# Kernel optimization log

Hardware: AMD Instinct MI355X
Metric: run time of the kernel (lower is better)

Reference implementation:

```python
import jax, jax.numpy as jnp
import numpy as np

B, N, DIM = 16, 1024, 768


def setup_inputs() -> dict:
    key = jax.random.key(0)
    ks = jax.random.split(key, 8)
    x = jax.random.normal(ks[0], (B, N, DIM), dtype=jnp.float32)
    y = jax.random.normal(ks[1], (B, N, DIM), dtype=jnp.float32)
    coords = jax.random.normal(ks[2], (N, N, 6), dtype=jnp.float32)
    # orthogonal init for U (as in torch init.orthogonal_)
    a = jax.random.normal(ks[3], (DIM, DIM), dtype=jnp.float32)
    q, r = jnp.linalg.qr(a)
    U = q * jnp.sign(jnp.diagonal(r))[None, :]
    S1 = jnp.ones((DIM,), dtype=jnp.float32)
    S2 = jnp.ones((DIM,), dtype=jnp.float32)
    gating = jnp.asarray(1.0, dtype=jnp.float32)
    temp = jnp.asarray(0.1, dtype=jnp.float32)
    pos_emb = jnp.zeros((N, 6, 1), dtype=jnp.float32)
    return {"x": x, "y": y, "coords": coords, "U": U, "S1": S1, "S2": S2,
            "gating": gating, "temp": temp, "pos_emb": pos_emb}


def reference(x, y, coords, U, S1, S2, gating, temp, pos_emb):
    dim = x.shape[-1]
    scale = dim ** (-0.5)
    # spectral decomposition: x @ U^T @ diag(S^2) @ U
    xu = x @ U.T                                   # [B,N,d]
    x1 = (xu * jnp.square(S1)) @ U                 # [B,N,d]
    x2 = (xu * jnp.square(S2)) @ U                 # [B,N,d]
    xs = jnp.stack([x1, x2], axis=1)               # [B,2,N,d]
    patch_score = jax.nn.softmax(
        jnp.einsum('bknd,bmd->bknm', xs, y) * scale, axis=-1)  # [B,2,N,M]
    pos = jnp.squeeze(coords @ pos_emb, -1)        # [N,M]
    pos_score = jax.nn.softmax(pos, axis=-1)[None, None]        # [1,1,N,M]
    g = jax.nn.sigmoid(gating)
    attn = (1.0 - g) * patch_score + g * pos_score  # [B,2,N,M]
    # entropy-routed gating
    entropy = jnp.sum(-attn * jnp.log(attn + 1e-8), axis=-1)    # [B,2,N]
    hmap = 2.0 - 2.0 * jax.nn.sigmoid(temp * jnp.transpose(entropy, (0, 2, 1)))  # [B,N,2]
    fgbg = hmap[..., 0] >= hmap[..., 1]
    route = jax.lax.stop_gradient(
        jnp.stack([fgbg, ~fgbg], axis=-1).astype(hmap.dtype))   # [B,N,2]
    heat_map = jnp.sum(hmap * route, axis=-1, keepdims=True)    # [B,N,1]
    attn_c = jnp.sum(attn * jnp.transpose(route, (0, 2, 1))[..., None], axis=1)  # [B,N,M]
    out = attn_c @ y                               # [B,N,d]
    return (out, heat_map)
```

## Files before the change

### kernel.cpp

```cpp
#include <hip/hip_runtime.h>
#include <hip/hip_bf16.h>

#define DEV __device__ __forceinline__

typedef unsigned short u16;
typedef short short8 __attribute__((ext_vector_type(8)));
typedef u16 u16x4 __attribute__((ext_vector_type(4)));
typedef float f32x16 __attribute__((ext_vector_type(16)));

static const int BB = 16;
static const int NN = 1024;
static const int DD = 768;

DEV u16 f2bf(float f) {
    unsigned u = __builtin_bit_cast(unsigned, f);
    unsigned r = u + 0x7fffu + ((u >> 16) & 1u);
    return (u16)(r >> 16);
}
DEV float h2f(u16 u) { return (float)__builtin_bit_cast(_Float16, u); }
DEV u16 f2h(float f) { return __builtin_bit_cast(u16, (_Float16)f); }

DEV void gl_lds16(const void* g, void* l) {
    __builtin_amdgcn_global_load_lds(
        (const __attribute__((address_space(1))) unsigned int*)g,
        (__attribute__((address_space(3))) unsigned int*)l, 16, 0, 0);
}

DEV void fence_bar() {
    asm volatile("" ::: "memory");
    __builtin_amdgcn_s_barrier();
    asm volatile("" ::: "memory");
}
DEV void wait_vm4() { asm volatile("s_waitcnt vmcnt(4)" ::: "memory"); }

template<int OM>
__global__ __launch_bounds__(256, 3) void gemm128(
    const u16* __restrict__ Ag, const u16* __restrict__ Bg, void* __restrict__ Cg,
    int K, int N, int zmod,
    long sA0, long sA1, long sB0, long sB1, long sC0, long sC1,
    float scale)
{
    __shared__ u16 As[128 * 64];
    __shared__ u16 Bs[128 * 64];

    int z = blockIdx.z;
    const u16* A = Ag + (long)(z % zmod) * sA0 + (long)(z / zmod) * sA1;
    const u16* B = Bg + (long)(z % zmod) * sB0 + (long)(z / zmod) * sB1;
    u16*   Cu = (u16*)Cg   + (long)(z % zmod) * sC0 + (long)(z / zmod) * sC1;
    float* Cf = (float*)Cg + (long)(z % zmod) * sC0 + (long)(z / zmod) * sC1;

    int tid  = threadIdx.x;
    int lane = tid & 63, wave = tid >> 6;
    int wm = wave & 1, wn = wave >> 1;
    int ln31 = lane & 31, khalf = lane >> 5;

    long m0 = (long)blockIdx.x * 128;
    long n0 = (long)blockIdx.y * 128;

    long aOfs[4], bOfs[4];
    u16 *lA[4], *lB[4];
#pragma unroll
    for (int i = 0; i < 4; i++) {
        int p = tid + i * 256;
        int row = p >> 3, qs = p & 7;
        int q = qs ^ (row & 7);
        aOfs[i] = (m0 + row) * (long)K + q * 8;
        bOfs[i] = (n0 + row) * (long)K + q * 8;
        lA[i] = As + p * 8;
        lB[i] = Bs + p * 8;
    }

    int aoff[2][4], boff[2][4];
#pragma unroll
    for (int t = 0; t < 2; t++) {
        int ra = wm * 64 + t * 32 + ln31;
        int rb = wn * 64 + t * 32 + ln31;
#pragma unroll
        for (int h = 0; h < 4; h++) {
            aoff[t][h] = ra * 64 + (((h * 2 + khalf) ^ (ra & 7)) * 8);
            boff[t][h] = rb * 64 + (((h * 2 + khalf) ^ (rb & 7)) * 8);
        }
    }

    f32x16 acc[2][2] = {};

    for (int k0 = 0; k0 < K; k0 += 64) {
#pragma unroll
        for (int i = 0; i < 4; i++) gl_lds16(A + aOfs[i] + k0, lA[i]);
#pragma unroll
        for (int i = 0; i < 4; i++) gl_lds16(B + bOfs[i] + k0, lB[i]);
        __syncthreads();

#pragma unroll
        for (int h = 0; h < 4; h++) {
            short8 af[2], bfr[2];
#pragma unroll
            for (int t = 0; t < 2; t++) af[t]  = *(const short8*)(As + aoff[t][h]);
#pragma unroll
            for (int t = 0; t < 2; t++) bfr[t] = *(const short8*)(Bs + boff[t][h]);
#pragma unroll
            for (int ti = 0; ti < 2; ti++)
#pragma unroll
                for (int tj = 0; tj < 2; tj++)
                    acc[ti][tj] = __builtin_amdgcn_mfma_f32_32x32x16_bf16(
                        af[ti], bfr[tj], acc[ti][tj], 0, 0, 0);
        }
        __syncthreads();
    }

    long crow = m0 + wm * 64 + 4 * khalf;
    long ccol = n0 + wn * 64 + ln31;
#pragma unroll
    for (int ti = 0; ti < 2; ti++)
#pragma unroll
        for (int tj = 0; tj < 2; tj++)
#pragma unroll
            for (int r = 0; r < 16; r++) {
                long row = crow + ti * 32 + (r & 3) + 8 * (r >> 2);
                long col = ccol + tj * 32;
                float v = acc[ti][tj][r] * scale;
                long idx = row * (long)N + col;
                if constexpr (OM == 0)      Cu[idx] = f2bf(v);
                else if constexpr (OM == 1) Cu[idx] = f2h(v);
                else                        Cf[idx] = v;
            }
}

template<int OM>
__global__ __launch_bounds__(512, 2) void gemm256(
    const u16* __restrict__ Ag, const u16* __restrict__ Bg, void* __restrict__ Cg,
    int K, int N, int zmod,
    long sA0, long sA1, long sB0, long sB1, long sC0, long sC1,
    float scale, int swz)
{
    __shared__ u16 lds[2][4][8192];

    int bx = blockIdx.x, by = blockIdx.y, bz = blockIdx.z;
    if (swz) {
        int gx = gridDim.x, gy = gridDim.y;
        int nwg = gx * gy * gridDim.z;
        int lin = bx + gx * (by + gy * bz);
        int sw = (lin & 7) * (nwg >> 3) + (lin >> 3);
        bx = sw % gx; int t = sw / gx;
        by = t % gy;  bz = t / gy;
    }

    int z = bz;
    const u16* A = Ag + (long)(z % zmod) * sA0 + (long)(z / zmod) * sA1;
    const u16* B = Bg + (long)(z % zmod) * sB0 + (long)(z / zmod) * sB1;
    u16*   Cu = (u16*)Cg   + (long)(z % zmod) * sC0 + (long)(z / zmod) * sC1;
    float* Cf = (float*)Cg + (long)(z % zmod) * sC0 + (long)(z / zmod) * sC1;

    int tid  = threadIdx.x;
    int lane = tid & 63, wave = tid >> 6;
    int wm = wave >> 2, wn = wave & 3;
    int ln31 = lane & 31, khalf = lane >> 5;

    long m0 = (long)bx * 256;
    long n0 = (long)by * 256;
    const u16* Apan = A + m0 * (long)K;
    const u16* Bpan = B + n0 * (long)K;

    long stA[2];
#pragma unroll
    for (int r = 0; r < 2; r++) {
        int p = tid + r * 512;
        int row = p >> 2, c = (p & 3) ^ ((row >> 1) & 3);
        stA[r] = (long)row * K + c * 8;
    }

    int aoffs[4][2], boffs[2][2];
#pragma unroll
    for (int m = 0; m < 4; m++) {
        int rr = wm * 128 + m * 32 + ln31;
#pragma unroll
        for (int sl = 0; sl < 2; sl++)
            aoffs[m][sl] = rr * 32 + (((sl * 2 + khalf) ^ ((rr >> 1) & 3)) * 8);
    }
#pragma unroll
    for (int n = 0; n < 2; n++) {
        int cc = wn * 64 + n * 32 + ln31;
#pragma unroll
        for (int sl = 0; sl < 2; sl++)
            boffs[n][sl] = cc * 32 + (((sl * 2 + khalf) ^ ((cc >> 1) & 3)) * 8);
    }

    f32x16 acc[4][2] = {};

    int nkt = K >> 6;
    int niter = nkt >> 1;

#define STG(PAN, BUF, HSEL, KT, KH) do {                                   \
    const u16* _s0 = (PAN) + stA[0] + (long)(KT) * 64 + (KH) * 32;         \
    const u16* _s1 = (PAN) + stA[1] + (long)(KT) * 64 + (KH) * 32;         \
    u16* _d = &lds[BUF][HSEL][0] + tid * 8;                                \
    gl_lds16(_s0, _d);                                                     \
    gl_lds16(_s1, _d + 4096);                                              \
} while (0)

#define PH(BUF, S, DOSTG, GUARD) do {                                      \
    short8 av[4], bv[2];                                                   \
    _Pragma("unroll")                                                      \
    for (int m = 0; m < 4; m++)                                            \
        av[m] = *(const short8*)(&lds[BUF][(S) >> 1][aoffs[m][(S) & 1]]);  \
    _Pragma("unroll")                                                      \
    for (int n = 0; n < 2; n++)                                            \
        bv[n] = *(const short8*)(&lds[BUF][2 + ((S) >> 1)][boffs[n][(S) & 1]]); \
    DOSTG;                                                                 \
    if (GUARD) wait_vm4();                                                 \
    fence_bar();                                                           \
    __builtin_amdgcn_s_setprio(1);                                         \
    _Pragma("unroll")                                                      \
    for (int m = 0; m < 4; m++)                                            \
        _Pragma("unroll")                                                  \
        for (int n = 0; n < 2; n++)                                        \
            acc[m][n] = __builtin_amdgcn_mfma_f32_32x32x16_bf16(           \
                av[m], bv[n], acc[m][n], 0, 0, 0);                         \
    __builtin_amdgcn_s_setprio(0);                                         \
    fence_bar();                                                           \
} while (0)

    STG(Apan, 0, 0, 0, 0);
    STG(Bpan, 0, 2, 0, 0);
    STG(Apan, 0, 1, 0, 1);
    STG(Bpan, 0, 3, 0, 1);
    STG(Apan, 1, 0, 1, 0);
    STG(Bpan, 1, 2, 1, 0);
    wait_vm4();
    fence_bar();

    for (int it = 0; it < niter; ++it) {
        int t1 = 2 * it + 1;
        int t2 = 2 * it + 2; int t2c = t2 < nkt ? t2 : nkt - 1;
        int t3 = 2 * it + 3; int t3c = t3 < nkt ? t3 : nkt - 1;
        PH(0, 0, STG(Apan, 1, 1, t1,  1), false);
        PH(0, 1, STG(Bpan, 1, 3, t1,  1), false);
        PH(0, 2, STG(Apan, 0, 0, t2c, 0), false);
        PH(0, 3, STG(Bpan, 0, 2, t2c, 0), true);
        PH(1, 0, STG(Apan, 0, 1, t2c, 1), false);
        PH(1, 1, STG(Bpan, 0, 3, t2c, 1), false);
        PH(1, 2, STG(Apan, 1, 0, t3c, 0), false);
        PH(1, 3, STG(Bpan, 1, 2, t3c, 0), true);
    }
#undef PH
#undef STG

    long crow = m0 + wm * 128 + 4 * khalf;
    long ccol = n0 + wn * 64 + ln31;
#pragma unroll
    for (int m = 0; m < 4; m++)
#pragma unroll
        for (int n = 0; n < 2; n++)
#pragma unroll
            for (int r = 0; r < 16; r++) {
                long row = crow + m * 32 + (r & 3) + 8 * (r >> 2);
                long col = ccol + n * 32;
                float v = acc[m][n][r] * scale;
                long idx = row * (long)N + col;
                if constexpr (OM == 0)      Cu[idx] = f2bf(v);
                else if constexpr (OM == 1) Cu[idx] = f2h(v);
                else                        Cf[idx] = v;
            }
}

DEV float wave_red_max(float v) {
#pragma unroll
    for (int o = 32; o; o >>= 1) v = fmaxf(v, __shfl_xor(v, o));
    return v;
}
DEV float wave_red_sum(float v) {
#pragma unroll
    for (int o = 32; o; o >>= 1) v += __shfl_xor(v, o);
    return v;
}
DEV float block_red_max(float v, float* sh) {
    v = wave_red_max(v);
    if ((threadIdx.x & 63) == 0) sh[threadIdx.x >> 6] = v;
    __syncthreads();
    v = fmaxf(fmaxf(sh[0], sh[1]), fmaxf(sh[2], sh[3]));
    __syncthreads();
    return v;
}
DEV float block_red_sum(float v, float* sh) {
    v = wave_red_sum(v);
    if ((threadIdx.x & 63) == 0) sh[threadIdx.x >> 6] = v;
    __syncthreads();
    v = (sh[0] + sh[1]) + (sh[2] + sh[3]);
    __syncthreads();
    return v;
}

__global__ __launch_bounds__(256) void k_prep_all(
    const float* __restrict__ x, const float* __restrict__ y,
    const float* __restrict__ coords, const float* __restrict__ U,
    const float* __restrict__ S1, const float* __restrict__ S2,
    const float* __restrict__ pe,
    u16* __restrict__ xb, u16* __restrict__ yb, u16* __restrict__ yT,
    u16* __restrict__ UTb, u16* __restrict__ VT1, u16* __restrict__ VT2,
    float* __restrict__ P)
{
    __shared__ float shmem[32 * 33];
    int bid = blockIdx.x, tid = threadIdx.x;

    if (bid < 12288) {
        float (*tile)[33] = (float(*)[33])shmem;
        int b = bid / 768, rem = bid % 768;
        int d0 = (rem % 24) * 32, m0 = (rem / 24) * 32;
        int r = tid >> 3, c4 = (tid & 7) * 4;
        const float* ybase = y + (long)b * NN * DD;
        float4 v = *(const float4*)(ybase + (long)(m0 + r) * DD + d0 + c4);
        u16x4 w4;
        w4[0] = f2bf(v.x); w4[1] = f2bf(v.y); w4[2] = f2bf(v.z); w4[3] = f2bf(v.w);
        *(u16x4*)(yb + (long)b * NN * DD + (long)(m0 + r) * DD + d0 + c4) = w4;
        tile[r][c4 + 0] = v.x; tile[r][c4 + 1] = v.y;
        tile[r][c4 + 2] = v.z; tile[r][c4 + 3] = v.w;
        __syncthreads();
        int d = tid >> 3, mq = (tid & 7) * 4;
        u16x4 o;
        o[0] = f2bf(tile[mq + 0][d]); o[1] = f2bf(tile[mq + 1][d]);
        o[2] = f2bf(tile[mq + 2][d]); o[3] = f2bf(tile[mq + 3][d]);
        *(u16x4*)(yT + (long)b * DD * NN + (long)(d0 + d) * NN + m0 + mq) = o;
        return;
    }
    bid -= 12288;

    if (bid < 6144) {
        long base = ((long)bid * 256 + tid) * 8;
        float4 f0 = *(const float4*)(x + base);
        float4 f1 = *(const float4*)(x + base + 4);
        short8 w;
        w[0] = (short)f2bf(f0.x); w[1] = (short)f2bf(f0.y);
        w[2] = (short)f2bf(f0.z); w[3] = (short)f2bf(f0.w);
        w[4] = (short)f2bf(f1.x); w[5] = (short)f2bf(f1.y);
        w[6] = (short)f2bf(f1.z); w[7] = (short)f2bf(f1.w);
        *(short8*)(xb + base) = w;
        return;
    }
    bid -= 6144;

    if (bid < 1024) {
        int n = bid, t = tid;
        float p6[6];
#pragma unroll
        for (int c = 0; c < 6; c++) p6[c] = pe[n * 6 + c];
        const float* cp0 = coords + ((long)n * NN + t * 4) * 6;
        float f[24];
#pragma unroll
        for (int qv = 0; qv < 6; qv++) {
            float4 q = *(const float4*)(cp0 + qv * 4);
            f[qv * 4 + 0] = q.x; f[qv * 4 + 1] = q.y;
            f[qv * 4 + 2] = q.z; f[qv * 4 + 3] = q.w;
        }
        float v[4];
#pragma unroll
        for (int i = 0; i < 4; i++) {
            v[i] = p6[0]*f[i*6+0] + p6[1]*f[i*6+1] + p6[2]*f[i*6+2]
                 + p6[3]*f[i*6+3] + p6[4]*f[i*6+4] + p6[5]*f[i*6+5];
        }
        float mx = block_red_max(fmaxf(fmaxf(v[0], v[1]), fmaxf(v[2], v[3])), shmem);
        float e[4], s = 0.f;
#pragma unroll
        for (int i = 0; i < 4; i++) { e[i] = __expf(v[i] - mx); s += e[i]; }
        float Z = block_red_sum(s, shmem);
        float inv = 1.f / Z;
        float4 o; o.x = e[0]*inv; o.y = e[1]*inv; o.z = e[2]*inv; o.w = e[3]*inv;
        *(float4*)(P + ((long)n << 10) + t * 4) = o;
        return;
    }
    bid -= 1024;

    {
        float (*tile)[33] = (float(*)[33])shmem;
        int i0 = (bid % 24) * 32, j0 = (bid / 24) * 32;
        int tx = tid & 31, ty = tid >> 5;
#pragma unroll
        for (int r = 0; r < 32; r += 8) {
            int i = i0 + ty + r, j = j0 + tx;
            tile[ty + r][tx] = U[(long)i * DD + j];
        }
        __syncthreads();
        float s1v = S1[i0 + tx];
        float s2v = S2[i0 + tx];
        s1v *= s1v; s2v *= s2v;
#pragma unroll
        for (int r = 0; r < 32; r += 8) {
            int j = j0 + ty + r, i = i0 + tx;
            float v = tile[tx][ty + r];
            UTb[(long)j * DD + i] = f2bf(v);
            VT1[(long)j * DD + i] = f2bf(s1v * v);
            VT2[(long)j * DD + i] = f2bf(s2v * v);
        }
    }
}

__global__ __launch_bounds__(128) void k_route(
    u16* __restrict__ S, const float* __restrict__ P,
    const float* __restrict__ gating, const float* __restrict__ temp,
    float* __restrict__ heat)
{
    int bn = (blockIdx.x << 1) | (threadIdx.x >> 6);
    int t = threadIdx.x & 63;
    int b = bn >> 10, n = bn & 1023;
    u16* s1p = S + ((long)(b * 2) << 20) + ((long)n << 10);
    u16* s2p = s1p + (1L << 20);
    const float* pp = P + ((long)n << 10);

    short8 r1a = *(const short8*)(s1p + t * 8);
    short8 r1b = *(const short8*)(s1p + 512 + t * 8);
    short8 r2a = *(const short8*)(s2p + t * 8);
    short8 r2b = *(const short8*)(s2p + 512 + t * 8);
    float4 pv0 = *(const float4*)(pp + t * 8);
    float4 pv1 = *(const float4*)(pp + t * 8 + 4);
    float4 pv2 = *(const float4*)(pp + 512 + t * 8);
    float4 pv3 = *(const float4*)(pp + 512 + t * 8 + 4);

    float s1[16], s2[16], p8[16];
#pragma unroll
    for (int i = 0; i < 8; i++) {
        s1[i]     = h2f((u16)r1a[i]);
        s1[i + 8] = h2f((u16)r1b[i]);
        s2[i]     = h2f((u16)r2a[i]);
        s2[i + 8] = h2f((u16)r2b[i]);
    }
    p8[0]=pv0.x;  p8[1]=pv0.y;  p8[2]=pv0.z;  p8[3]=pv0.w;
    p8[4]=pv1.x;  p8[5]=pv1.y;  p8[6]=pv1.z;  p8[7]=pv1.w;
    p8[8]=pv2.x;  p8[9]=pv2.y;  p8[10]=pv2.z; p8[11]=pv2.w;
    p8[12]=pv3.x; p8[13]=pv3.y; p8[14]=pv3.z; p8[15]=pv3.w;

    float m1 = s1[0], m2 = s2[0];
#pragma unroll
    for (int i = 1; i < 16; i++) { m1 = fmaxf(m1, s1[i]); m2 = fmaxf(m2, s2[i]); }
    float mx1 = wave_red_max(m1);
    float mx2 = wave_red_max(m2);

    float e1[16], e2[16], z1 = 0.f, z2 = 0.f;
#pragma unroll
    for (int i = 0; i < 16; i++) {
        e1[i] = __expf(s1[i] - mx1); z1 += e1[i];
        e2[i] = __expf(s2[i] - mx2); z2 += e2[i];
    }
    float Z1 = wave_red_sum(z1);
    float Z2 = wave_red_sum(z2);

    float g = 1.f / (1.f + __expf(-gating[0]));
    float c1 = (1.f - g) / Z1, c2 = (1.f - g) / Z2;

    float a1[16], a2[16], hh1 = 0.f, hh2 = 0.f;
#pragma unroll
    for (int i = 0; i < 16; i++) {
        a1[i] = e1[i] * c1 + g * p8[i];
        a2[i] = e2[i] * c2 + g * p8[i];
        hh1 -= a1[i] * __logf(a1[i] + 1e-8f);
        hh2 -= a2[i] * __logf(a2[i] + 1e-8f);
    }
    float H1 = wave_red_sum(hh1);
    float H2 = wave_red_sum(hh2);

    float tv = temp[0];
    float hm0 = 2.f - 2.f / (1.f + __expf(-tv * H1));
    float hm1 = 2.f - 2.f / (1.f + __expf(-tv * H2));
    int ks = (hm0 >= hm1) ? 0 : 1;
    if (t == 0) heat[bn] = ks ? hm1 : hm0;

    short8 w0, w1;
#pragma unroll
    for (int i = 0; i < 8; i++) {
        w0[i] = (short)f2bf(ks ? a2[i] : a1[i]);
        w1[i] = (short)f2bf(ks ? a2[i + 8] : a1[i + 8]);
    }
    *(short8*)(s1p + t * 8) = w0;
    *(short8*)(s1p + 512 + t * 8) = w1;
}

extern "C" void kernel_launch(void* const* d_in, const int* in_sizes, int n_in,
                              void* d_out, int out_size, void* d_ws, size_t ws_size,
                              hipStream_t stream)
{
    (void)in_sizes; (void)n_in; (void)out_size; (void)ws_size;
    const float* x      = (const float*)d_in[0];
    const float* y      = (const float*)d_in[1];
    const float* coords = (const float*)d_in[2];
    const float* U      = (const float*)d_in[3];
    const float* S1     = (const float*)d_in[4];
    const float* S2     = (const float*)d_in[5];
    const float* gating = (const float*)d_in[6];
    const float* temp   = (const float*)d_in[7];
    const float* pose   = (const float*)d_in[8];

    float* out  = (float*)d_out;
    float* heat = out + (long)BB * NN * DD;

    char* w = (char*)d_ws;
    u16* UTb = (u16*)w;  w += (long)DD * DD * 2;
    u16* VT  = (u16*)w;  w += (long)2 * DD * DD * 2;
    u16* W2  = (u16*)w;  w += (long)2 * DD * DD * 2;
    u16* x12 = (u16*)w;  w += (long)2 * BB * NN * DD * 2;
    u16* yb  = (u16*)w;  w += (long)BB * NN * DD * 2;
    u16* yT  = (u16*)w;  w += (long)BB * DD * NN * 2;
    u16* S   = (u16*)w;  w += (long)BB * 2 * NN * NN * 2;
    float* P = (float*)w;

    u16* xb = S;

    const long MBN = (long)BB * NN * DD;
    const long BND = (long)NN * DD;
    const long SPL = (long)NN * NN;
    const long DSQ = (long)DD * DD;

    k_prep_all<<<dim3(20032), dim3(256), 0, stream>>>(
        x, y, coords, U, S1, S2, pose, xb, yb, yT, UTb, VT, VT + DSQ, P);

    gemm128<0><<<dim3(DD / 128, DD / 128, 2), dim3(256), 0, stream>>>(
        UTb, VT, W2, DD, DD, 2,
        0L, 0L, DSQ, 0L, DSQ, 0L, 1.0f);

    gemm256<0><<<dim3(BB * NN / 256, DD / 256, 1), dim3(512), 0, stream>>>(
        xb, W2, x12, DD, DD, 1,
        0L, 0L, 0L, 0L, 0L, 0L, 1.0f, 0);
    gemm256<0><<<dim3(BB * NN / 256, DD / 256, 1), dim3(512), 0, stream>>>(
        xb, W2 + DSQ, x12 + MBN, DD, DD, 1,
        0L, 0L, 0L, 0L, 0L, 0L, 1.0f, 0);

    gemm256<1><<<dim3(NN / 256, NN / 256, BB), dim3(512), 0, stream>>>(
        x12, yb, S, DD, NN, 2,
        MBN, BND, 0L, BND, SPL, 2 * SPL, 0.036084391824351615f, 1);
    gemm256<1><<<dim3(NN / 256, NN / 256, BB), dim3(512), 0, stream>>>(
        x12 + 8 * BND, yb + 8 * BND, S + 16 * SPL, DD, NN, 2,
        MBN, BND, 0L, BND, SPL, 2 * SPL, 0.036084391824351615f, 1);

    k_route<<<dim3(BB * NN / 2), dim3(128), 0, stream>>>(S, P, gating, temp, heat);

    gemm128<2><<<dim3(NN / 128, DD / 128, BB), dim3(256), 0, stream>>>(
        S, yT, out, NN, DD, 1,
        0L, 2 * SPL, 0L, BND, 0L, BND, 1.0f);
}
```

Before: 372.0 us.

## Widen prep tiles, merge split GEMM launches, use 256 tile for final GEMM

The y transpose and convert step now uses 64x64 tiles with 8-wide vector loads and stores, and the x conversion handles 16 elements per thread, which cuts the prep block count. The two x12 GEMM launches are merged into one batched launch, as are the two score GEMM launches. The final attention-times-y GEMM moves from the 128 tile kernel to the 256 tile kernel. The aim is less launch overhead and tail waste, and better per-block data reuse. The cost is fewer blocks for the smaller output GEMM and a larger LDS footprint in the prep kernel. It also depends on gemm256 supporting mode 2 and the batch stride layout the merged launches assume.

Result: no change. 366.2 us (-1.6%).

```diff
diff --git a/kernel.cpp b/kernel.cpp
--- a/kernel.cpp
+++ b/kernel.cpp
@@ -299,44 +299,67 @@
     u16* __restrict__ UTb, u16* __restrict__ VT1, u16* __restrict__ VT2,
     float* __restrict__ P)
 {
-    __shared__ float shmem[32 * 33];
+    __shared__ float shmem[64 * 65];
     int bid = blockIdx.x, tid = threadIdx.x;
 
-    if (bid < 12288) {
-        float (*tile)[33] = (float(*)[33])shmem;
-        int b = bid / 768, rem = bid % 768;
-        int d0 = (rem % 24) * 32, m0 = (rem / 24) * 32;
-        int r = tid >> 3, c4 = (tid & 7) * 4;
+    if (bid < 3072) {
+        float (*tile)[65] = (float(*)[65])shmem;
+        int b = bid / 192, rem = bid % 192;
+        int d0 = (rem % 12) * 64, m0 = (rem / 12) * 64;
+        int lr = tid >> 3, lc = (tid & 7) * 8;
         const float* ybase = y + (long)b * NN * DD;
-        float4 v = *(const float4*)(ybase + (long)(m0 + r) * DD + d0 + c4);
-        u16x4 w4;
-        w4[0] = f2bf(v.x); w4[1] = f2bf(v.y); w4[2] = f2bf(v.z); w4[3] = f2bf(v.w);
-        *(u16x4*)(yb + (long)b * NN * DD + (long)(m0 + r) * DD + d0 + c4) = w4;
-        tile[r][c4 + 0] = v.x; tile[r][c4 + 1] = v.y;
-        tile[r][c4 + 2] = v.z; tile[r][c4 + 3] = v.w;
+        u16* ybb = yb + (long)b * NN * DD;
+#pragma unroll
+        for (int rr = 0; rr < 64; rr += 32) {
+            int m = m0 + lr + rr;
+            const float* src = ybase + (long)m * DD + d0 + lc;
+            float4 v0 = *(const float4*)src;
+            float4 v1 = *(const float4*)(src + 4);
+            short8 w;
+            w[0] = (short)f2bf(v0.x); w[1] = (short)f2bf(v0.y);
+            w[2] = (short)f2bf(v0.z); w[3] = (short)f2bf(v0.w);
+            w[4] = (short)f2bf(v1.x); w[5] = (short)f2bf(v1.y);
+            w[6] = (short)f2bf(v1.z); w[7] = (short)f2bf(v1.w);
+            *(short8*)(ybb + (long)m * DD + d0 + lc) = w;
+            float* tp = &tile[lr + rr][lc];
+            tp[0] = v0.x; tp[1] = v0.y; tp[2] = v0.z; tp[3] = v0.w;
+            tp[4] = v1.x; tp[5] = v1.y; tp[6] = v1.z; tp[7] = v1.w;
+        }
         __syncthreads();
-        int d = tid >> 3, mq = (tid & 7) * 4;
-        u16x4 o;
-        o[0] = f2bf(tile[mq + 0][d]); o[1] = f2bf(tile[mq + 1][d]);
-        o[2] = f2bf(tile[mq + 2][d]); o[3] = f2bf(tile[mq + 3][d]);
-        *(u16x4*)(yT + (long)b * DD * NN + (long)(d0 + d) * NN + m0 + mq) = o;
+        int td = tid >> 3, tm = (tid & 7) * 8;
+        u16* yTb = yT + (long)b * DD * NN;
+#pragma unroll
+        for (int dd = 0; dd < 64; dd += 32) {
+            int d = d0 + td + dd;
+            short8 o;
+#pragma unroll
+            for (int j = 0; j < 8; j++) o[j] = (short)f2bf(tile[tm + j][td + dd]);
+            *(short8*)(yTb + (long)d * NN + m0 + tm) = o;
+        }
         return;
     }
-    bid -= 12288;
-
-    if (bid < 6144) {
-        long base = ((long)bid * 256 + tid) * 8;
+    bid -= 3072;
+
+    if (bid < 3072) {
+        long base = ((long)bid * 256 + tid) * 16;
         float4 f0 = *(const float4*)(x + base);
         float4 f1 = *(const float4*)(x + base + 4);
-        short8 w;
-        w[0] = (short)f2bf(f0.x); w[1] = (short)f2bf(f0.y);
-        w[2] = (short)f2bf(f0.z); w[3] = (short)f2bf(f0.w);
-        w[4] = (short)f2bf(f1.x); w[5] = (short)f2bf(f1.y);
-        w[6] = (short)f2bf(f1.z); w[7] = (short)f2bf(f1.w);
-        *(short8*)(xb + base) = w;
+        float4 f2 = *(const float4*)(x + base + 8);
+        float4 f3 = *(const float4*)(x + base + 12);
+        short8 w0, w1;
+        w0[0] = (short)f2bf(f0.x); w0[1] = (short)f2bf(f0.y);
+        w0[2] = (short)f2bf(f0.z); w0[3] = (short)f2bf(f0.w);
+        w0[4] = (short)f2bf(f1.x); w0[5] = (short)f2bf(f1.y);
+        w0[6] = (short)f2bf(f1.z); w0[7] = (short)f2bf(f1.w);
+        w1[0] = (short)f2bf(f2.x); w1[1] = (short)f2bf(f2.y);
+        w1[2] = (short)f2bf(f2.z); w1[3] = (short)f2bf(f2.w);
+        w1[4] = (short)f2bf(f3.x); w1[5] = (short)f2bf(f3.y);
+        w1[6] = (short)f2bf(f3.z); w1[7] = (short)f2bf(f3.w);
+        *(short8*)(xb + base) = w0;
+        *(short8*)(xb + base + 8) = w1;
         return;
     }
-    bid -= 6144;
+    bid -= 3072;
 
     if (bid < 1024) {
         int n = bid, t = tid;
@@ -507,30 +530,24 @@
     const long SPL = (long)NN * NN;
     const long DSQ = (long)DD * DD;
 
-    k_prep_all<<<dim3(20032), dim3(256), 0, stream>>>(
+    k_prep_all<<<dim3(7744), dim3(256), 0, stream>>>(
         x, y, coords, U, S1, S2, pose, xb, yb, yT, UTb, VT, VT + DSQ, P);
 
     gemm128<0><<<dim3(DD / 128, DD / 128, 2), dim3(256), 0, stream>>>(
         UTb, VT, W2, DD, DD, 2,
         0L, 0L, DSQ, 0L, DSQ, 0L, 1.0f);
 
-    gemm256<0><<<dim3(BB * NN / 256, DD / 256, 1), dim3(512), 0, stream>>>(
-        xb, W2, x12, DD, DD, 1,
-        0L, 0L, 0L, 0L, 0L, 0L, 1.0f, 0);
-    gemm256<0><<<dim3(BB * NN / 256, DD / 256, 1), dim3(512), 0, stream>>>(
-        xb, W2 + DSQ, x12 + MBN, DD, DD, 1,
-        0L, 0L, 0L, 0L, 0L, 0L, 1.0f, 0);
-
-    gemm256<1><<<dim3(NN / 256, NN / 256, BB), dim3(512), 0, stream>>>(
+    gemm256<0><<<dim3(BB * NN / 256, DD / 256, 2), dim3(512), 0, stream>>>(
+        xb, W2, x12, DD, DD, 2,
+        0L, 0L, DSQ, 0L, MBN, 0L, 1.0f, 0);
+
+    gemm256<1><<<dim3(NN / 256, NN / 256, BB * 2), dim3(512), 0, stream>>>(
         x12, yb, S, DD, NN, 2,
         MBN, BND, 0L, BND, SPL, 2 * SPL, 0.036084391824351615f, 1);
-    gemm256<1><<<dim3(NN / 256, NN / 256, BB), dim3(512), 0, stream>>>(
-        x12 + 8 * BND, yb + 8 * BND, S + 16 * SPL, DD, NN, 2,
-        MBN, BND, 0L, BND, SPL, 2 * SPL, 0.036084391824351615f, 1);
 
     k_route<<<dim3(BB * NN / 2), dim3(128), 0, stream>>>(S, P, gating, temp, heat);
 
-    gemm128<2><<<dim3(NN / 128, DD / 128, BB), dim3(256), 0, stream>>>(
+    gemm256<2><<<dim3(NN / 256, DD / 256, BB), dim3(512), 0, stream>>>(
         S, yT, out, NN, DD, 1,
-        0L, 2 * SPL, 0L, BND, 0L, BND, 1.0f);
-}
+        0L, 2 * SPL, 0L, BND, 0L, BND, 1.0f, 1);
+}
```
